# Kernel optimization log

Measured on AMD Instinct MI355X. Metric: run time of the kernel, lower is better.

The kernel has to match this reference:

```python
import jax, jax.numpy as jnp
import numpy as np

DIM = 1024
NUM_HEADS = 16
HEAD_DIM = DIM // NUM_HEADS
MLP_HIDDEN = 4 * DIM
SCALE = HEAD_DIM ** -0.5
EPS = 1e-5


def setup_inputs() -> dict:
    key = jax.random.key(0)
    ks = jax.random.split(key, 6)
    s = (2.0 / DIM) ** 0.5
    sd = (2.0 / MLP_HIDDEN) ** 0.5
    return {
        "x": jax.random.normal(ks[0], (2, 2048, DIM), dtype=jnp.float32),
        "attn_qkv_weight": jax.random.normal(ks[1], (3 * DIM, DIM), dtype=jnp.float32) * s,
        "attn_out_weight": jax.random.normal(ks[2], (DIM, DIM), dtype=jnp.float32) * s,
        "norm1_weight": jnp.ones((DIM,), jnp.float32),
        "norm1_bias": jnp.zeros((DIM,), jnp.float32),
        "mlp_gate_weight": jax.random.normal(ks[3], (MLP_HIDDEN, DIM), dtype=jnp.float32) * s,
        "mlp_up_weight": jax.random.normal(ks[4], (MLP_HIDDEN, DIM), dtype=jnp.float32) * s,
        "mlp_down_weight": jax.random.normal(ks[5], (DIM, MLP_HIDDEN), dtype=jnp.float32) * sd,
        "norm2_weight": jnp.ones((DIM,), jnp.float32),
        "norm2_bias": jnp.zeros((DIM,), jnp.float32),
    }


def _layer_norm(x, w, b):
    mean = x.mean(axis=-1, keepdims=True)
    var = jnp.mean(jnp.square(x - mean), axis=-1, keepdims=True)
    return (x - mean) / jnp.sqrt(var + EPS) * w + b


def reference(x, attn_qkv_weight, attn_out_weight, norm1_weight, norm1_bias,
              mlp_gate_weight, mlp_up_weight, mlp_down_weight, norm2_weight, norm2_bias):
    B, S, D = x.shape
    residual1 = x
    xn = _layer_norm(x, norm1_weight, norm1_bias)
    qkv = xn @ attn_qkv_weight.T                      # [B,S,3D]
    qkv = qkv.reshape(B, S, 3, NUM_HEADS, HEAD_DIM).transpose(2, 0, 3, 1, 4)
    q, k, v = qkv[0], qkv[1], qkv[2]                  # [B,H,S,hd]
    scores = jnp.einsum('bhqd,bhkd->bhqk', q, k) * SCALE  # full O(S^2) matrix
    attn = jax.nn.softmax(scores, axis=-1)            # no causal mask (default False)
    out = jnp.einsum('bhqk,bhkd->bhqd', attn, v)      # [B,H,S,hd]
    out = out.transpose(0, 2, 1, 3).reshape(B, S, D)
    x2 = residual1 + out @ attn_out_weight.T
    xn2 = _layer_norm(x2, norm2_weight, norm2_bias)
    gate = xn2 @ mlp_gate_weight.T
    up = xn2 @ mlp_up_weight.T
    hidden = jax.nn.silu(gate) * up
    return x2 + hidden @ mlp_down_weight.T
```

## Files before the change

kernel.cpp:

```cpp
#include <hip/hip_runtime.h>

typedef float f32x4 __attribute__((ext_vector_type(4)));
typedef __bf16 bf16x8 __attribute__((ext_vector_type(8)));
typedef unsigned int u32;

#define DEV __device__ __forceinline__
#define WAITVM(n) asm volatile("s_waitcnt vmcnt(" #n ")" ::: "memory")

DEV void gload_lds16(const void* g, void* l) {
  __builtin_amdgcn_global_load_lds(
      (const __attribute__((address_space(1))) u32*)g,
      (__attribute__((address_space(3))) u32*)l, 16, 0, 0);
}

DEV int xcd_swz(int flat, int nwg) {
  return (flat & 7) * (nwg >> 3) + (flat >> 3);
}

__global__ __launch_bounds__(256) void cvt_bf16(const float* __restrict__ in,
                                                __bf16* __restrict__ o, int n) {
  int i = (blockIdx.x * 256 + threadIdx.x) * 8;
  if (i >= n) return;
  float4 a = *(const float4*)(in + i);
  float4 b = *(const float4*)(in + i + 4);
  union { bf16x8 v; __bf16 e[8]; } u;
  u.e[0] = (__bf16)a.x; u.e[1] = (__bf16)a.y; u.e[2] = (__bf16)a.z; u.e[3] = (__bf16)a.w;
  u.e[4] = (__bf16)b.x; u.e[5] = (__bf16)b.y; u.e[6] = (__bf16)b.z; u.e[7] = (__bf16)b.w;
  *(bf16x8*)(o + i) = u.v;
}

__global__ __launch_bounds__(256) void ln_kernel(const float* __restrict__ x,
                                                 const float* __restrict__ w,
                                                 const float* __restrict__ b,
                                                 __bf16* __restrict__ o) {
  const int row = blockIdx.x, tid = threadIdx.x;
  const float4 v = ((const float4*)(x + (size_t)row * 1024))[tid];
  float s  = v.x + v.y + v.z + v.w;
  float s2 = v.x * v.x + v.y * v.y + v.z * v.z + v.w * v.w;
  for (int off = 32; off; off >>= 1) {
    s  += __shfl_down(s, off);
    s2 += __shfl_down(s2, off);
  }
  __shared__ float rs[4], rs2[4];
  if ((tid & 63) == 0) { rs[tid >> 6] = s; rs2[tid >> 6] = s2; }
  __syncthreads();
  float S = rs[0] + rs[1] + rs[2] + rs[3];
  float S2 = rs2[0] + rs2[1] + rs2[2] + rs2[3];
  float mean = S * (1.0f / 1024.0f);
  float var = S2 * (1.0f / 1024.0f) - mean * mean;
  float inv = rsqrtf(var + 1e-5f);
  const float4 wv = ((const float4*)w)[tid];
  const float4 bv = ((const float4*)b)[tid];
  union { ushort4 u4; __bf16 e[4]; } u;
  u.e[0] = (__bf16)((v.x - mean) * inv * wv.x + bv.x);
  u.e[1] = (__bf16)((v.y - mean) * inv * wv.y + bv.y);
  u.e[2] = (__bf16)((v.z - mean) * inv * wv.z + bv.z);
  u.e[3] = (__bf16)((v.w - mean) * inv * wv.w + bv.w);
  *(ushort4*)(o + (size_t)row * 1024 + tid * 4) = u.u4;
}


template <int EPI, int MI>
__global__ __launch_bounds__(256) void gemm_bt(const __bf16* __restrict__ A,
                                               const __bf16* __restrict__ B,
                                               void* __restrict__ Cout,
                                               const float* __restrict__ Res,
                                               int M, int N, int K) {
  constexpr int BM = MI * 32;
  __shared__ __align__(16) __bf16 As[3][BM * 32];
  __shared__ __align__(16) __bf16 Bs[3][128 * 32];
  const int tid = threadIdx.x;
  const int lane = tid & 63;
  const int w = tid >> 6;
  const int wr = w >> 1, wc = w & 1;
  const int l15 = lane & 15, g = lane >> 4;
  const int c8 = ((g + (l15 >> 1)) & 3) * 8;

  const int nbx = gridDim.x;
  const int logical = xcd_swz(blockIdx.y * nbx + blockIdx.x, nbx * gridDim.y);
  const int per = 8 * nbx, grp = logical / per, rem = logical % per;
  const int bm = (grp * 8 + (rem & 7)) * BM;
  const int bn = (rem >> 3) * 128;

  f32x4 acc[MI][4] = {};

  auto stage = [&](int buf, int k0) {
#pragma unroll
    for (int p = 0; p < MI / 2; ++p) {
      const int ch = p * 256 + tid;
      const int row = ch >> 2;
      const int gc = ((ch & 3) - ((ch >> 3) & 3)) & 3;
      gload_lds16(A + (size_t)(bm + row) * K + k0 + gc * 8,
                  &As[buf][(p * 256 + w * 64) * 8]);
    }
#pragma unroll
    for (int p = 0; p < 2; ++p) {
      const int ch = p * 256 + tid;
      const int row = ch >> 2;
      const int gc = ((ch & 3) - ((ch >> 3) & 3)) & 3;
      gload_lds16(B + (size_t)(bn + row) * K + k0 + gc * 8,
                  &Bs[buf][(p * 256 + w * 64) * 8]);
    }
  };

  const int NT = K >> 5;
  stage(0, 0);
  stage(1, 32);

  int cur = 0;
  for (int t = 0; t < NT; ++t) {
    if (t + 1 < NT) {
      if constexpr (MI == 4) { WAITVM(4); } else { WAITVM(3); }
    } else {
      WAITVM(0);
    }
    __builtin_amdgcn_s_barrier();
    if (t + 2 < NT) {
      int sb = cur + 2; if (sb >= 3) sb -= 3;
      stage(sb, (t + 2) * 32);
    }
    bf16x8 af[MI], bfr[4];
#pragma unroll
    for (int i = 0; i < MI; ++i)
      af[i] = *(const bf16x8*)(&As[cur][(wr * (MI * 16) + i * 16 + l15) * 32 + c8]);
#pragma unroll
    for (int j = 0; j < 4; ++j)
      bfr[j] = *(const bf16x8*)(&Bs[cur][(wc * 64 + j * 16 + l15) * 32 + c8]);
#pragma unroll
    for (int i = 0; i < MI; ++i)
#pragma unroll
      for (int j = 0; j < 4; ++j)
        acc[i][j] = __builtin_amdgcn_mfma_f32_16x16x32_bf16(af[i], bfr[j], acc[i][j], 0, 0, 0);
    cur = (cur == 2) ? 0 : cur + 1;
  }

  const int r0 = bm + wr * (MI * 16) + g * 4;
  const int c0 = bn + wc * 64 + l15;
#pragma unroll
  for (int i = 0; i < MI; ++i)
#pragma unroll
    for (int j = 0; j < 4; ++j)
#pragma unroll
      for (int r = 0; r < 4; ++r) {
        const size_t idx = (size_t)(r0 + i * 16 + r) * N + (c0 + j * 16);
        const float v = acc[i][j][r];
        if (EPI == 0) ((__bf16*)Cout)[idx] = (__bf16)v;
        else          ((float*)Cout)[idx] = v + Res[idx];
      }
}

__global__ __launch_bounds__(256, 2) void gemm_mlp(const __bf16* __restrict__ A,
                                                   const __bf16* __restrict__ BG,
                                                   const __bf16* __restrict__ BU,
                                                   __bf16* __restrict__ H,
                                                   int M, int N, int K) {
  __shared__ __align__(16) __bf16 As[3][128 * 32];
  __shared__ __align__(16) __bf16 Bg[3][128 * 32];
  __shared__ __align__(16) __bf16 Bu[3][128 * 32];
  const int tid = threadIdx.x;
  const int lane = tid & 63;
  const int w = tid >> 6;
  const int wr = w >> 1, wc = w & 1;
  const int l15 = lane & 15, g = lane >> 4;
  const int c8 = ((g + (l15 >> 1)) & 3) * 8;

  const int nbx = gridDim.x;
  const int logical = xcd_swz(blockIdx.y * nbx + blockIdx.x, nbx * gridDim.y);
  const int per = 8 * nbx, grp = logical / per, rem = logical % per;
  const int bm = (grp * 8 + (rem & 7)) * 128;
  const int bn = (rem >> 3) * 128;

  f32x4 accg[4][4] = {};
  f32x4 accu[4][4] = {};

  auto stage = [&](int buf, int k0) {
#pragma unroll
    for (int p = 0; p < 2; ++p) {
      const int ch = p * 256 + tid;
      const int row = ch >> 2;
      const int gc = ((ch & 3) - ((ch >> 3) & 3)) & 3;
      const int coff = gc * 8;
      const int dst = (p * 256 + w * 64) * 8;
      gload_lds16(A + (size_t)(bm + row) * K + k0 + coff, &As[buf][dst]);
      gload_lds16(BG + (size_t)(bn + row) * K + k0 + coff, &Bg[buf][dst]);
      gload_lds16(BU + (size_t)(bn + row) * K + k0 + coff, &Bu[buf][dst]);
    }
  };

  const int NT = K >> 5;
  stage(0, 0);
  stage(1, 32);

  int cur = 0;
  for (int t = 0; t < NT; ++t) {
    if (t + 1 < NT) { WAITVM(6); } else { WAITVM(0); }
    __builtin_amdgcn_s_barrier();
    if (t + 2 < NT) {
      int sb = cur + 2; if (sb >= 3) sb -= 3;
      stage(sb, (t + 2) * 32);
    }
    bf16x8 af[4], bgf[4], buf_[4];
#pragma unroll
    for (int i = 0; i < 4; ++i)
      af[i] = *(const bf16x8*)(&As[cur][(wr * 64 + i * 16 + l15) * 32 + c8]);
#pragma unroll
    for (int j = 0; j < 4; ++j) {
      bgf[j] = *(const bf16x8*)(&Bg[cur][(wc * 64 + j * 16 + l15) * 32 + c8]);
      buf_[j] = *(const bf16x8*)(&Bu[cur][(wc * 64 + j * 16 + l15) * 32 + c8]);
    }
#pragma unroll
    for (int i = 0; i < 4; ++i)
#pragma unroll
      for (int j = 0; j < 4; ++j) {
        accg[i][j] = __builtin_amdgcn_mfma_f32_16x16x32_bf16(af[i], bgf[j], accg[i][j], 0, 0, 0);
        accu[i][j] = __builtin_amdgcn_mfma_f32_16x16x32_bf16(af[i], buf_[j], accu[i][j], 0, 0, 0);
      }
    cur = (cur == 2) ? 0 : cur + 1;
  }

  const int r0 = bm + wr * 64 + g * 4;
  const int c0 = bn + wc * 64 + l15;
#pragma unroll
  for (int i = 0; i < 4; ++i)
#pragma unroll
    for (int j = 0; j < 4; ++j)
#pragma unroll
      for (int r = 0; r < 4; ++r) {
        const float gt = accg[i][j][r];
        const float ut = accu[i][j][r];
        const float h = gt / (1.0f + __expf(-gt)) * ut;
        H[(size_t)(r0 + i * 16 + r) * N + (c0 + j * 16)] = (__bf16)h;
      }
}

__global__ __launch_bounds__(256) void transpose_v(const __bf16* __restrict__ qkv,
                                                   __bf16* __restrict__ vT) {
  const int st = blockIdx.x, bh = blockIdx.y;
  const int b = bh >> 4, h = bh & 15;
  __shared__ __bf16 tile[64][80];
  const int tid = threadIdx.x;
#pragma unroll
  for (int it = 0; it < 2; ++it) {
    const int idx = it * 256 + tid;
    const int r = idx >> 3, c0 = (idx & 7) * 8;
    bf16x8 v = *(const bf16x8*)(qkv + (size_t)(b * 2048 + st * 64 + r) * 3072 + 2048 + h * 64 + c0);
    *(bf16x8*)&tile[r][c0] = v;
  }
  __syncthreads();
#pragma unroll
  for (int it = 0; it < 2; ++it) {
    const int idx = it * 256 + tid;
    const int d = idx >> 3, s0 = (idx & 7) * 8;
    union { bf16x8 v; __bf16 e[8]; } u;
#pragma unroll
    for (int j = 0; j < 8; ++j) u.e[j] = tile[s0 + j][d];
    *(bf16x8*)(vT + (size_t)(bh * 64 + d) * 2048 + st * 64 + s0) = u.v;
  }
}

__global__ __launch_bounds__(256) void attn_kernel(const __bf16* __restrict__ qkv,
                                                   const __bf16* __restrict__ vT,
                                                   __bf16* __restrict__ outp) {
  const int logical = xcd_swz(blockIdx.y * 32 + blockIdx.x, 1024);
  const int qt = logical & 31, bh = logical >> 5;
  const int b = bh >> 4, h = bh & 15;
  const int tid = threadIdx.x, lane = tid & 63, w = tid >> 6;
  const int l15 = lane & 15, g = lane >> 4;
  const float CSC = 0.125f * 1.44269504f;

  __shared__ __align__(16) __bf16 Ks[64 * 64];
  __shared__ __align__(16) __bf16 Vs[64 * 64];
  __shared__ __align__(16) __bf16 Ps[4][16 * 80];

  const int qrow = qt * 64 + w * 16 + l15;
  const size_t qbase = (size_t)(b * 2048 + qrow) * 3072 + h * 64;
  bf16x8 qf0, qf1;
  {
    union { bf16x8 v; __bf16 e[8]; } a, bqq, oa, ob;
    a.v = *(const bf16x8*)(qkv + qbase + g * 8);
    bqq.v = *(const bf16x8*)(qkv + qbase + 32 + g * 8);
#pragma unroll
    for (int j = 0; j < 8; ++j) {
      oa.e[j] = (__bf16)((float)a.e[j] * CSC);
      ob.e[j] = (__bf16)((float)bqq.e[j] * CSC);
    }
    qf0 = oa.v; qf1 = ob.v;
  }

  f32x4 o_acc[4] = {};
  float l_r[4] = {0.f, 0.f, 0.f, 0.f};

  const size_t kgbase = (size_t)(b * 2048) * 3072 + 1024 + h * 64;
  const size_t vgbase = (size_t)bh * 64 * 2048;

  float4 kreg[2], vreg[2];
  auto issue = [&](int t) {
    const int kv0 = t * 64;
#pragma unroll
    for (int p = 0; p < 2; ++p) {
      const int ch = p * 256 + w * 64 + lane;
      const int row = ch >> 3, c = ch & 7;
      const int gc = c ^ (row & 7);
      kreg[p] = *(const float4*)(qkv + kgbase + (size_t)(kv0 + row) * 3072 + gc * 8);
      vreg[p] = *(const float4*)(vT + vgbase + (size_t)row * 2048 + kv0 + gc * 8);
    }
  };
  auto commit = [&]() {
#pragma unroll
    for (int p = 0; p < 2; ++p) {
      *(float4*)(Ks + (p * 256 + w * 64) * 8 + lane * 8) = kreg[p];
      *(float4*)(Vs + (p * 256 + w * 64) * 8 + lane * 8) = vreg[p];
    }
  };

  issue(0);
  commit();
  __syncthreads();

  for (int t = 0; t < 32; ++t) {
    if (t + 1 < 32) issue(t + 1);

    f32x4 sf[4];
    __builtin_amdgcn_s_setprio(1);
#pragma unroll
    for (int ni = 0; ni < 4; ++ni) {
      const int krow = ni * 16 + l15;
      const __bf16* kb = Ks + krow * 64;
      const bf16x8 kf0 = *(const bf16x8*)(kb + ((g ^ (krow & 7)) * 8));
      const bf16x8 kf1 = *(const bf16x8*)(kb + (((4 + g) ^ (krow & 7)) * 8));
      f32x4 z = {0.f, 0.f, 0.f, 0.f};
      z = __builtin_amdgcn_mfma_f32_16x16x32_bf16(qf0, kf0, z, 0, 0, 0);
      z = __builtin_amdgcn_mfma_f32_16x16x32_bf16(qf1, kf1, z, 0, 0, 0);
      sf[ni] = z;
    }
    __builtin_amdgcn_s_setprio(0);

#pragma unroll
    for (int ni = 0; ni < 4; ++ni)
#pragma unroll
      for (int r = 0; r < 4; ++r) {
        const float pv = exp2f(sf[ni][r]);
        sf[ni][r] = pv;
        l_r[r] += pv;
      }

    __bf16* pw = Ps[w];
#pragma unroll
    for (int ni = 0; ni < 4; ++ni)
#pragma unroll
      for (int r = 0; r < 4; ++r) {
        const int row = g * 4 + r;
        const int pc = (ni * 2 + (l15 >> 3)) ^ (row & 7);
        pw[row * 80 + pc * 8 + (l15 & 7)] = (__bf16)sf[ni][r];
      }
    asm volatile("" ::: "memory");
    const bf16x8 pa0 = *(const bf16x8*)(pw + l15 * 80 + ((g ^ (l15 & 7)) * 8));
    const bf16x8 pa1 = *(const bf16x8*)(pw + l15 * 80 + (((4 + g) ^ (l15 & 7)) * 8));

    __builtin_amdgcn_s_setprio(1);
#pragma unroll
    for (int ni = 0; ni < 4; ++ni) {
      const int vrow = ni * 16 + l15;
      const __bf16* vb = Vs + vrow * 64;
      const bf16x8 vf0 = *(const bf16x8*)(vb + ((g ^ (vrow & 7)) * 8));
      const bf16x8 vf1 = *(const bf16x8*)(vb + (((4 + g) ^ (vrow & 7)) * 8));
      o_acc[ni] = __builtin_amdgcn_mfma_f32_16x16x32_bf16(pa0, vf0, o_acc[ni], 0, 0, 0);
      o_acc[ni] = __builtin_amdgcn_mfma_f32_16x16x32_bf16(pa1, vf1, o_acc[ni], 0, 0, 0);
    }
    __builtin_amdgcn_s_setprio(0);

    if (t + 1 < 32) {
      __syncthreads();
      commit();
      __syncthreads();
    }
  }

#pragma unroll
  for (int mk = 1; mk < 16; mk <<= 1)
#pragma unroll
    for (int r = 0; r < 4; ++r) l_r[r] += __shfl_xor(l_r[r], mk);
#pragma unroll
  for (int r = 0; r < 4; ++r) {
    const int orow = qt * 64 + w * 16 + g * 4 + r;
    const float invl = 1.0f / l_r[r];
#pragma unroll
    for (int ni = 0; ni < 4; ++ni)
      outp[(size_t)(b * 2048 + orow) * 1024 + h * 64 + ni * 16 + l15] =
          (__bf16)(o_acc[ni][r] * invl);
  }
}

extern "C" void kernel_launch(void* const* d_in, const int* in_sizes, int n_in,
                              void* d_out, int out_size, void* d_ws, size_t ws_size,
                              hipStream_t stream) {
  const float* x     = (const float*)d_in[0];
  const float* Wqkv  = (const float*)d_in[1];
  const float* Wout  = (const float*)d_in[2];
  const float* n1w   = (const float*)d_in[3];
  const float* n1b   = (const float*)d_in[4];
  const float* Wgate = (const float*)d_in[5];
  const float* Wup   = (const float*)d_in[6];
  const float* Wdown = (const float*)d_in[7];
  const float* n2w   = (const float*)d_in[8];
  const float* n2b   = (const float*)d_in[9];
  float* out = (float*)d_out;
  char* ws = (char*)d_ws;
  const size_t MB = 1u << 20;

  __bf16* XN  = (__bf16*)(ws + 0);
  __bf16* QKV = (__bf16*)(ws + 8 * MB);
  __bf16* VT  = (__bf16*)(ws + 32 * MB);
  __bf16* ATT = (__bf16*)(ws + 40 * MB);
  float*  X2  = (float*)(ws + 48 * MB);
  __bf16* H   = QKV;
  __bf16* WQ  = (__bf16*)(ws + 64 * MB);
  __bf16* WO  = (__bf16*)(ws + 70 * MB);
  __bf16* WG  = (__bf16*)(ws + 72 * MB);
  __bf16* WU  = (__bf16*)(ws + 80 * MB);
  __bf16* WD  = (__bf16*)(ws + 88 * MB);

  cvt_bf16<<<3145728 / 2048, 256, 0, stream>>>(Wqkv, WQ, 3145728);
  cvt_bf16<<<1048576 / 2048, 256, 0, stream>>>(Wout, WO, 1048576);
  cvt_bf16<<<4194304 / 2048, 256, 0, stream>>>(Wgate, WG, 4194304);
  cvt_bf16<<<4194304 / 2048, 256, 0, stream>>>(Wup, WU, 4194304);
  cvt_bf16<<<4194304 / 2048, 256, 0, stream>>>(Wdown, WD, 4194304);

  ln_kernel<<<4096, 256, 0, stream>>>(x, n1w, n1b, XN);
  gemm_bt<0, 4><<<dim3(24, 32), 256, 0, stream>>>(XN, WQ, QKV, nullptr, 4096, 3072, 1024);
  transpose_v<<<dim3(32, 32), 256, 0, stream>>>(QKV, VT);
  attn_kernel<<<dim3(32, 32), 256, 0, stream>>>(QKV, VT, ATT);
  gemm_bt<1, 2><<<dim3(8, 64), 256, 0, stream>>>(ATT, WO, X2, x, 4096, 1024, 1024);
  ln_kernel<<<4096, 256, 0, stream>>>(X2, n2w, n2b, XN);
  gemm_mlp<<<dim3(32, 32), 256, 0, stream>>>(XN, WG, WU, H, 4096, 4096, 1024);
  gemm_bt<1, 2><<<dim3(8, 64), 256, 0, stream>>>(H, WD, out, X2, 4096, 1024, 4096);

  (void)in_sizes; (void)n_in; (void)out_size; (void)ws_size;
}
```

Measured before the change: 376.7 us.

## Split attention over two KV halves with merge kernel and batch weight conversion

After: 307.4 us, median of 3. 1.23x faster.

```diff
diff --git a/kernel.cpp b/kernel.cpp
--- a/kernel.cpp
+++ b/kernel.cpp
@@ -17,16 +17,30 @@
   return (flat & 7) * (nwg >> 3) + (flat >> 3);
 }
 
-__global__ __launch_bounds__(256) void cvt_bf16(const float* __restrict__ in,
-                                                __bf16* __restrict__ o, int n) {
-  int i = (blockIdx.x * 256 + threadIdx.x) * 8;
-  if (i >= n) return;
-  float4 a = *(const float4*)(in + i);
-  float4 b = *(const float4*)(in + i + 4);
+__global__ __launch_bounds__(256) void cvt_all(const float* __restrict__ s0,
+                                               const float* __restrict__ s1,
+                                               const float* __restrict__ s2,
+                                               const float* __restrict__ s3,
+                                               const float* __restrict__ s4,
+                                               __bf16* __restrict__ d0,
+                                               __bf16* __restrict__ d1,
+                                               __bf16* __restrict__ d2,
+                                               __bf16* __restrict__ d3,
+                                               __bf16* __restrict__ d4) {
+  size_t i = ((size_t)blockIdx.x * 256 + threadIdx.x) * 8;
+  const float* s; __bf16* d; size_t off;
+  if (i < 3145728)        { s = s0; d = d0; off = 0; }
+  else if (i < 4194304)   { s = s1; d = d1; off = 3145728; }
+  else if (i < 8388608)   { s = s2; d = d2; off = 4194304; }
+  else if (i < 12582912)  { s = s3; d = d3; off = 8388608; }
+  else                    { s = s4; d = d4; off = 12582912; }
+  const size_t j = i - off;
+  float4 a = *(const float4*)(s + j);
+  float4 b = *(const float4*)(s + j + 4);
   union { bf16x8 v; __bf16 e[8]; } u;
   u.e[0] = (__bf16)a.x; u.e[1] = (__bf16)a.y; u.e[2] = (__bf16)a.z; u.e[3] = (__bf16)a.w;
   u.e[4] = (__bf16)b.x; u.e[5] = (__bf16)b.y; u.e[6] = (__bf16)b.z; u.e[7] = (__bf16)b.w;
-  *(bf16x8*)(o + i) = u.v;
+  *(bf16x8*)(d + j) = u.v;
 }
 
 __global__ __launch_bounds__(256) void ln_kernel(const float* __restrict__ x,
@@ -260,9 +274,12 @@
 
 __global__ __launch_bounds__(256) void attn_kernel(const __bf16* __restrict__ qkv,
                                                    const __bf16* __restrict__ vT,
-                                                   __bf16* __restrict__ outp) {
-  const int logical = xcd_swz(blockIdx.y * 32 + blockIdx.x, 1024);
-  const int qt = logical & 31, bh = logical >> 5;
+                                                   __bf16* __restrict__ Opart,
+                                                   float* __restrict__ Lpart) {
+  const int logical = xcd_swz(blockIdx.y * 32 + blockIdx.x, 2048);
+  const int qt = logical & 31;
+  const int rest = logical >> 5;
+  const int bh = rest >> 1, half = rest & 1;
   const int b = bh >> 4, h = bh & 15;
   const int tid = threadIdx.x, lane = tid & 63, w = tid >> 6;
   const int l15 = lane & 15, g = lane >> 4;
@@ -276,13 +293,13 @@
   const size_t qbase = (size_t)(b * 2048 + qrow) * 3072 + h * 64;
   bf16x8 qf0, qf1;
   {
-    union { bf16x8 v; __bf16 e[8]; } a, bqq, oa, ob;
+    union { bf16x8 v; __bf16 e[8]; } a, bq, oa, ob;
     a.v = *(const bf16x8*)(qkv + qbase + g * 8);
-    bqq.v = *(const bf16x8*)(qkv + qbase + 32 + g * 8);
+    bq.v = *(const bf16x8*)(qkv + qbase + 32 + g * 8);
 #pragma unroll
     for (int j = 0; j < 8; ++j) {
       oa.e[j] = (__bf16)((float)a.e[j] * CSC);
-      ob.e[j] = (__bf16)((float)bqq.e[j] * CSC);
+      ob.e[j] = (__bf16)((float)bq.e[j] * CSC);
     }
     qf0 = oa.v; qf1 = ob.v;
   }
@@ -293,32 +310,18 @@
   const size_t kgbase = (size_t)(b * 2048) * 3072 + 1024 + h * 64;
   const size_t vgbase = (size_t)bh * 64 * 2048;
 
-  float4 kreg[2], vreg[2];
-  auto issue = [&](int t) {
-    const int kv0 = t * 64;
+  for (int tt = 0; tt < 16; ++tt) {
+    const int kv0 = half * 1024 + tt * 64;
 #pragma unroll
     for (int p = 0; p < 2; ++p) {
       const int ch = p * 256 + w * 64 + lane;
       const int row = ch >> 3, c = ch & 7;
       const int gc = c ^ (row & 7);
-      kreg[p] = *(const float4*)(qkv + kgbase + (size_t)(kv0 + row) * 3072 + gc * 8);
-      vreg[p] = *(const float4*)(vT + vgbase + (size_t)row * 2048 + kv0 + gc * 8);
-    }
-  };
-  auto commit = [&]() {
-#pragma unroll
-    for (int p = 0; p < 2; ++p) {
-      *(float4*)(Ks + (p * 256 + w * 64) * 8 + lane * 8) = kreg[p];
-      *(float4*)(Vs + (p * 256 + w * 64) * 8 + lane * 8) = vreg[p];
-    }
-  };
-
-  issue(0);
-  commit();
-  __syncthreads();
-
-  for (int t = 0; t < 32; ++t) {
-    if (t + 1 < 32) issue(t + 1);
+      gload_lds16(qkv + kgbase + (size_t)(kv0 + row) * 3072 + gc * 8, Ks + (p * 256 + w * 64) * 8);
+      gload_lds16(vT + vgbase + (size_t)row * 2048 + kv0 + gc * 8, Vs + (p * 256 + w * 64) * 8);
+    }
+    WAITVM(0);
+    __syncthreads();
 
     f32x4 sf[4];
     __builtin_amdgcn_s_setprio(1);
@@ -368,27 +371,40 @@
       o_acc[ni] = __builtin_amdgcn_mfma_f32_16x16x32_bf16(pa1, vf1, o_acc[ni], 0, 0, 0);
     }
     __builtin_amdgcn_s_setprio(0);
-
-    if (t + 1 < 32) {
-      __syncthreads();
-      commit();
-      __syncthreads();
-    }
+    __syncthreads();
   }
 
 #pragma unroll
   for (int mk = 1; mk < 16; mk <<= 1)
 #pragma unroll
     for (int r = 0; r < 4; ++r) l_r[r] += __shfl_xor(l_r[r], mk);
+
+  const size_t obase = (size_t)half * 4194304;
 #pragma unroll
   for (int r = 0; r < 4; ++r) {
     const int orow = qt * 64 + w * 16 + g * 4 + r;
-    const float invl = 1.0f / l_r[r];
+    const size_t grow = (size_t)(b * 2048 + orow);
+    if (l15 == 0) Lpart[half * 65536 + grow * 16 + h] = l_r[r];
 #pragma unroll
     for (int ni = 0; ni < 4; ++ni)
-      outp[(size_t)(b * 2048 + orow) * 1024 + h * 64 + ni * 16 + l15] =
-          (__bf16)(o_acc[ni][r] * invl);
-  }
+      Opart[obase + grow * 1024 + h * 64 + ni * 16 + l15] = (__bf16)o_acc[ni][r];
+  }
+}
+
+__global__ __launch_bounds__(256) void attn_merge(const __bf16* __restrict__ Opart,
+                                                  const float* __restrict__ Lpart,
+                                                  __bf16* __restrict__ outp) {
+  const int row = blockIdx.x, tid = threadIdx.x;
+  const int col = tid * 4, h = tid >> 4;
+  const float l = Lpart[row * 16 + h] + Lpart[65536 + row * 16 + h];
+  const float inv = 1.0f / l;
+  union { ushort4 u; __bf16 e[4]; } a, b, o;
+  a.u = *(const ushort4*)(Opart + (size_t)row * 1024 + col);
+  b.u = *(const ushort4*)(Opart + 4194304 + (size_t)row * 1024 + col);
+#pragma unroll
+  for (int j = 0; j < 4; ++j)
+    o.e[j] = (__bf16)(((float)a.e[j] + (float)b.e[j]) * inv);
+  *(ushort4*)(outp + (size_t)row * 1024 + col) = o.u;
 }
 
 extern "C" void kernel_launch(void* const* d_in, const int* in_sizes, int n_in,
@@ -413,23 +429,23 @@
   __bf16* VT  = (__bf16*)(ws + 32 * MB);
   __bf16* ATT = (__bf16*)(ws + 40 * MB);
   float*  X2  = (float*)(ws + 48 * MB);
+  __bf16* OP  = (__bf16*)(ws + 48 * MB);
   __bf16* H   = QKV;
   __bf16* WQ  = (__bf16*)(ws + 64 * MB);
+  float*  LP  = (float*)(ws + 64 * MB);
   __bf16* WO  = (__bf16*)(ws + 70 * MB);
   __bf16* WG  = (__bf16*)(ws + 72 * MB);
   __bf16* WU  = (__bf16*)(ws + 80 * MB);
   __bf16* WD  = (__bf16*)(ws + 88 * MB);
 
-  cvt_bf16<<<3145728 / 2048, 256, 0, stream>>>(Wqkv, WQ, 3145728);
-  cvt_bf16<<<1048576 / 2048, 256, 0, stream>>>(Wout, WO, 1048576);
-  cvt_bf16<<<4194304 / 2048, 256, 0, stream>>>(Wgate, WG, 4194304);
-  cvt_bf16<<<4194304 / 2048, 256, 0, stream>>>(Wup, WU, 4194304);
-  cvt_bf16<<<4194304 / 2048, 256, 0, stream>>>(Wdown, WD, 4194304);
+  cvt_all<<<16777216 / 2048, 256, 0, stream>>>(Wqkv, Wout, Wgate, Wup, Wdown,
+                                               WQ, WO, WG, WU, WD);
 
   ln_kernel<<<4096, 256, 0, stream>>>(x, n1w, n1b, XN);
   gemm_bt<0, 4><<<dim3(24, 32), 256, 0, stream>>>(XN, WQ, QKV, nullptr, 4096, 3072, 1024);
   transpose_v<<<dim3(32, 32), 256, 0, stream>>>(QKV, VT);
-  attn_kernel<<<dim3(32, 32), 256, 0, stream>>>(QKV, VT, ATT);
+  attn_kernel<<<dim3(32, 64), 256, 0, stream>>>(QKV, VT, OP, LP);
+  attn_merge<<<4096, 256, 0, stream>>>(OP, LP, ATT);
   gemm_bt<1, 2><<<dim3(8, 64), 256, 0, stream>>>(ATT, WO, X2, x, 4096, 1024, 1024);
   ln_kernel<<<4096, 256, 0, stream>>>(X2, n2w, n2b, XN);
   gemm_mlp<<<dim3(32, 32), 256, 0, stream>>>(XN, WG, WU, H, 4096, 4096, 1024);
```
